# Optimization experiments

Measured on AMD Instinct MI355X. Metric: run time of the kernel, lower is better.

Reference implementation:

```python
import jax, jax.numpy as jnp
import numpy as np

N = 50000
E = 800000
IN_C, HID, OUT_C = 512, 256, 128


def gcn_conv(x, edge_index, W, b, num_nodes):
    # PyG GCNConv: add self-loops, symmetric normalization, linear-then-aggregate.
    h = x @ W  # [N, out]
    src = jnp.concatenate([edge_index[0], jnp.arange(num_nodes)])
    dst = jnp.concatenate([edge_index[1], jnp.arange(num_nodes)])
    ones = jnp.ones(src.shape[0], dtype=x.dtype)
    deg = jax.ops.segment_sum(ones, dst, num_segments=num_nodes)  # in-degree incl. self-loop
    dinv = jax.lax.rsqrt(deg)  # deg >= 1 thanks to self-loops
    norm = dinv[src] * dinv[dst]  # [E+N]
    msg = h[src] * norm[:, None]  # gather + scale
    out = jax.ops.segment_sum(msg, dst, num_segments=num_nodes)  # scatter-add
    return out + b


def setup_inputs() -> dict:
    key = jax.random.key(0)
    k_x, k_e, k_w1, k_b1, k_w2, k_b2 = jax.random.split(key, 6)
    x = jax.random.normal(k_x, (N, IN_C), dtype=jnp.float32)
    edge_index = jax.random.randint(k_e, (2, E), 0, N, dtype=jnp.int64)
    s1 = 1.0 / np.sqrt(IN_C)
    s2 = 1.0 / np.sqrt(HID)
    W1 = jax.random.uniform(k_w1, (IN_C, HID), jnp.float32, -s1, s1)
    b1 = jax.random.uniform(k_b1, (HID,), jnp.float32, -s1, s1)
    W2 = jax.random.uniform(k_w2, (HID, OUT_C), jnp.float32, -s2, s2)
    b2 = jax.random.uniform(k_b2, (OUT_C,), jnp.float32, -s2, s2)
    return {"x": x, "edge_index": edge_index, "W1": W1, "b1": b1, "W2": W2, "b2": b2}


def reference(x, edge_index, W1, b1, W2, b2):
    h = gcn_conv(x, edge_index, W1, b1, N)
    h = jax.nn.relu(h)
    # dropout in eval mode == identity
    return gcn_conv(h, edge_index, W2, b2, N)
```

## Files before the change

### kernel.cpp

```cpp
#include <hip/hip_runtime.h>
#include <stdint.h>

typedef __bf16 bf16_t;
typedef bf16_t bf16x8 __attribute__((ext_vector_type(8)));
typedef bf16_t bf16x4 __attribute__((ext_vector_type(4)));
typedef bf16_t bf16x2 __attribute__((ext_vector_type(2)));
typedef float  f32x4  __attribute__((ext_vector_type(4)));

#define IN_C 512
#define HID  256
#define OUTC 128

__global__ void k_detect(const void* __restrict__ ei, int* __restrict__ flag, int n_nodes) {
  if (blockIdx.x == 0 && threadIdx.x == 0) {
    const long long* p = (const long long*)ei;
    int ok = 1;
    for (int i = 0; i < 64; ++i) {
      long long v = p[i];
      if (v < 0 || v >= n_nodes) ok = 0;
    }
    *flag = ok;
  }
}

__global__ void k_hist(const void* __restrict__ ei, const int* __restrict__ flag,
                       int* __restrict__ cnt, int E) {
  int e = blockIdx.x * blockDim.x + threadIdx.x;
  if (e >= E) return;
  int d;
  if (*flag) d = (int)((const long long*)ei)[(size_t)E + e];
  else       d = ((const int*)ei)[E + e];
  atomicAdd(&cnt[d], 1);
}

__global__ void k_scan1(const int* __restrict__ cnt, int* __restrict__ ex,
                        int* __restrict__ part, float* __restrict__ dinv, int n) {
  __shared__ int sh[256];
  int i = blockIdx.x * 256 + threadIdx.x;
  int v = (i < n) ? cnt[i] : 0;
  if (i < n) dinv[i] = rsqrtf((float)v + 1.0f);
  sh[threadIdx.x] = v;
  __syncthreads();
  int val = v;
  for (int off = 1; off < 256; off <<= 1) {
    int t = (threadIdx.x >= off) ? sh[threadIdx.x - off] : 0;
    __syncthreads();
    val += t;
    sh[threadIdx.x] = val;
    __syncthreads();
  }
  if (i < n) ex[i] = val - v;
  if (threadIdx.x == 255) part[blockIdx.x] = val;
}

__global__ void k_scan2(int* __restrict__ part, int nb) {
  __shared__ int sh[256];
  int v = (threadIdx.x < nb) ? part[threadIdx.x] : 0;
  sh[threadIdx.x] = v;
  __syncthreads();
  int val = v;
  for (int off = 1; off < 256; off <<= 1) {
    int t = (threadIdx.x >= off) ? sh[threadIdx.x - off] : 0;
    __syncthreads();
    val += t;
    sh[threadIdx.x] = val;
    __syncthreads();
  }
  if (threadIdx.x < nb) part[threadIdx.x] = val - v;
}

__global__ void k_scan3(int* __restrict__ rs, const int* __restrict__ part,
                        int* __restrict__ cur, int n, int Etot) {
  int i = blockIdx.x * 256 + threadIdx.x;
  if (i < n) {
    int r = rs[i] + part[blockIdx.x];
    rs[i] = r;
    cur[i] = r;
  }
  if (i == 0) rs[n] = Etot;
}

__global__ void k_fill(const void* __restrict__ ei, const int* __restrict__ flag,
                       int* __restrict__ cur, int* __restrict__ csr, int E) {
  int e = blockIdx.x * blockDim.x + threadIdx.x;
  if (e >= E) return;
  int s, d;
  if (*flag) {
    const long long* p = (const long long*)ei;
    s = (int)p[e];
    d = (int)p[(size_t)E + e];
  } else {
    const int* p = (const int*)ei;
    s = p[e];
    d = p[E + e];
  }
  int pos = atomicAdd(&cur[d], 1);
  csr[pos] = s;
}

__global__ void k_transw(const float* __restrict__ W1, const float* __restrict__ W2,
                         bf16_t* __restrict__ W1t, bf16_t* __restrict__ W2t) {
  int t = blockIdx.x * blockDim.x + threadIdx.x;
  if (t < IN_C * HID) {
    int k = t / HID, nn = t % HID;
    W1t[(size_t)nn * IN_C + k] = (bf16_t)W1[t];
  } else {
    int u = t - IN_C * HID;
    if (u < HID * OUTC) {
      int k = u / OUTC, nn = u % OUTC;
      W2t[(size_t)nn * HID + k] = (bf16_t)W2[u];
    }
  }
}

__global__ __launch_bounds__(256, 2) void k_gemm1(const float* __restrict__ x,
                                                  const bf16_t* __restrict__ Bt,
                                                  bf16_t* __restrict__ C, int n) {
  __shared__ bf16_t As[64 * 40];
  __shared__ bf16_t Bs[256 * 40];
  const int bm = blockIdx.x;
  const int tid = threadIdx.x;
  const int wave = tid >> 6, lane = tid & 63;
  const int wm = (wave >> 1) * 32, wn = (wave & 1) * 128;
  const int quad = lane >> 4, l16 = lane & 15;
  const int arow = tid >> 2, acol = (tid & 3) * 8;
  const int grow = bm * 64 + arow;

  f32x4 acc[2][8];
  for (int i = 0; i < 2; ++i)
    for (int j = 0; j < 8; ++j)
      for (int r = 0; r < 4; ++r) acc[i][j][r] = 0.0f;

  for (int kk = 0; kk < IN_C; kk += 32) {
    bf16x8 va;
    if (grow < n) {
      const float4* px = (const float4*)(x + (size_t)grow * IN_C + kk + acol);
      float4 a = px[0], b = px[1];
      va[0] = (bf16_t)a.x; va[1] = (bf16_t)a.y; va[2] = (bf16_t)a.z; va[3] = (bf16_t)a.w;
      va[4] = (bf16_t)b.x; va[5] = (bf16_t)b.y; va[6] = (bf16_t)b.z; va[7] = (bf16_t)b.w;
    } else {
      for (int i = 0; i < 8; ++i) va[i] = (bf16_t)0.0f;
    }
    *(bf16x8*)(&As[arow * 40 + acol]) = va;
#pragma unroll
    for (int c = 0; c < 4; ++c) {
      bf16x8 vb = *(const bf16x8*)(Bt + (size_t)tid * IN_C + kk + c * 8);
      *(bf16x8*)(&Bs[tid * 40 + c * 8]) = vb;
    }
    __syncthreads();
    bf16x8 af[2], bfr[8];
#pragma unroll
    for (int i = 0; i < 2; ++i)
      af[i] = *(const bf16x8*)(&As[(wm + i * 16 + l16) * 40 + quad * 8]);
#pragma unroll
    for (int j = 0; j < 8; ++j)
      bfr[j] = *(const bf16x8*)(&Bs[(wn + j * 16 + l16) * 40 + quad * 8]);
#pragma unroll
    for (int i = 0; i < 2; ++i)
#pragma unroll
      for (int j = 0; j < 8; ++j)
        acc[i][j] = __builtin_amdgcn_mfma_f32_16x16x32_bf16(af[i], bfr[j], acc[i][j], 0, 0, 0);
    __syncthreads();
  }

#pragma unroll
  for (int i = 0; i < 2; ++i) {
#pragma unroll
    for (int j = 0; j < 8; ++j) {
      int col = wn + j * 16 + l16;
      int row0 = bm * 64 + wm + i * 16 + quad * 4;
#pragma unroll
      for (int r = 0; r < 4; ++r)
        C[(size_t)(row0 + r) * HID + col] = (bf16_t)acc[i][j][r];
    }
  }
}

__global__ __launch_bounds__(256, 2) void k_gemm2(const bf16_t* __restrict__ A,
                                                  const bf16_t* __restrict__ Bt,
                                                  bf16_t* __restrict__ C) {
  __shared__ bf16_t As[64 * 40];
  __shared__ bf16_t Bs[128 * 40];
  const int bm = blockIdx.x;
  const int tid = threadIdx.x;
  const int wave = tid >> 6, lane = tid & 63;
  const int wm = (wave >> 1) * 32, wn = (wave & 1) * 64;
  const int quad = lane >> 4, l16 = lane & 15;
  const int arow = tid >> 2, acol = (tid & 3) * 8;
  const int brow = tid >> 1, bcol = (tid & 1) * 16;

  f32x4 acc[2][4];
  for (int i = 0; i < 2; ++i)
    for (int j = 0; j < 4; ++j)
      for (int r = 0; r < 4; ++r) acc[i][j][r] = 0.0f;

  for (int kk = 0; kk < HID; kk += 32) {
    bf16x8 va = *(const bf16x8*)(A + (size_t)(bm * 64 + arow) * HID + kk + acol);
    *(bf16x8*)(&As[arow * 40 + acol]) = va;
#pragma unroll
    for (int c = 0; c < 2; ++c) {
      bf16x8 vb = *(const bf16x8*)(Bt + (size_t)brow * HID + kk + bcol + c * 8);
      *(bf16x8*)(&Bs[brow * 40 + bcol + c * 8]) = vb;
    }
    __syncthreads();
    bf16x8 af[2], bfr[4];
#pragma unroll
    for (int i = 0; i < 2; ++i)
      af[i] = *(const bf16x8*)(&As[(wm + i * 16 + l16) * 40 + quad * 8]);
#pragma unroll
    for (int j = 0; j < 4; ++j)
      bfr[j] = *(const bf16x8*)(&Bs[(wn + j * 16 + l16) * 40 + quad * 8]);
#pragma unroll
    for (int i = 0; i < 2; ++i)
#pragma unroll
      for (int j = 0; j < 4; ++j)
        acc[i][j] = __builtin_amdgcn_mfma_f32_16x16x32_bf16(af[i], bfr[j], acc[i][j], 0, 0, 0);
    __syncthreads();
  }

#pragma unroll
  for (int i = 0; i < 2; ++i) {
#pragma unroll
    for (int j = 0; j < 4; ++j) {
      int col = wn + j * 16 + l16;
      int row0 = bm * 64 + wm + i * 16 + quad * 4;
#pragma unroll
      for (int r = 0; r < 4; ++r)
        C[(size_t)(row0 + r) * OUTC + col] = (bf16_t)acc[i][j][r];
    }
  }
}

__global__ void k_agg_l1(const bf16_t* __restrict__ H, const int* __restrict__ rs,
                         const int* __restrict__ csr, const float* __restrict__ dinv,
                         const float* __restrict__ b1, bf16_t* __restrict__ R,
                         int n, int mpad) {
  int d = blockIdx.x * 4 + (threadIdx.x >> 6);
  if (d >= mpad) return;
  int lane = threadIdx.x & 63;
  if (d >= n) {
    bf16x4 z;
    z[0] = (bf16_t)0.0f; z[1] = (bf16_t)0.0f; z[2] = (bf16_t)0.0f; z[3] = (bf16_t)0.0f;
    *(bf16x4*)(R + (size_t)d * HID + lane * 4) = z;
    return;
  }
  int e0 = rs[d], e1 = rs[d + 1];
  float acc[4][4];
  for (int k = 0; k < 4; ++k)
    for (int c = 0; c < 4; ++c) acc[k][c] = 0.f;
  int e = e0;
  for (; e + 4 <= e1; e += 4) {
    int s0 = csr[e], s1 = csr[e + 1], s2 = csr[e + 2], s3 = csr[e + 3];
    float w0 = dinv[s0], w1 = dinv[s1], w2 = dinv[s2], w3 = dinv[s3];
    bf16x4 h0 = *(const bf16x4*)(H + (size_t)s0 * HID + lane * 4);
    bf16x4 h1 = *(const bf16x4*)(H + (size_t)s1 * HID + lane * 4);
    bf16x4 h2 = *(const bf16x4*)(H + (size_t)s2 * HID + lane * 4);
    bf16x4 h3 = *(const bf16x4*)(H + (size_t)s3 * HID + lane * 4);
#pragma unroll
    for (int c = 0; c < 4; ++c) {
      acc[0][c] += w0 * (float)h0[c];
      acc[1][c] += w1 * (float)h1[c];
      acc[2][c] += w2 * (float)h2[c];
      acc[3][c] += w3 * (float)h3[c];
    }
  }
  for (; e < e1; ++e) {
    int s0 = csr[e];
    float w0 = dinv[s0];
    bf16x4 h0 = *(const bf16x4*)(H + (size_t)s0 * HID + lane * 4);
#pragma unroll
    for (int c = 0; c < 4; ++c) acc[0][c] += w0 * (float)h0[c];
  }
  float dd = dinv[d];
  float dv2 = dd * dd;
  bf16x4 hs = *(const bf16x4*)(H + (size_t)d * HID + lane * 4);
  float4 bb = ((const float4*)b1)[lane];
  float a0 = acc[0][0] + acc[1][0] + acc[2][0] + acc[3][0];
  float a1 = acc[0][1] + acc[1][1] + acc[2][1] + acc[3][1];
  float a2 = acc[0][2] + acc[1][2] + acc[2][2] + acc[3][2];
  float a3 = acc[0][3] + acc[1][3] + acc[2][3] + acc[3][3];
  float v0 = fmaxf(a0 * dd + dv2 * (float)hs[0] + bb.x, 0.f);
  float v1 = fmaxf(a1 * dd + dv2 * (float)hs[1] + bb.y, 0.f);
  float v2 = fmaxf(a2 * dd + dv2 * (float)hs[2] + bb.z, 0.f);
  float v3 = fmaxf(a3 * dd + dv2 * (float)hs[3] + bb.w, 0.f);
  bf16x4 o;
  o[0] = (bf16_t)v0; o[1] = (bf16_t)v1; o[2] = (bf16_t)v2; o[3] = (bf16_t)v3;
  *(bf16x4*)(R + (size_t)d * HID + lane * 4) = o;
}

__global__ void k_agg_l2(const bf16_t* __restrict__ H, const int* __restrict__ rs,
                         const int* __restrict__ csr, const float* __restrict__ dinv,
                         const float* __restrict__ b2, float* __restrict__ out, int n) {
  int d = blockIdx.x * 4 + (threadIdx.x >> 6);
  if (d >= n) return;
  int lane = threadIdx.x & 63;
  int e0 = rs[d], e1 = rs[d + 1];
  float acc[4][2];
  for (int k = 0; k < 4; ++k) { acc[k][0] = 0.f; acc[k][1] = 0.f; }
  int e = e0;
  for (; e + 4 <= e1; e += 4) {
    int s0 = csr[e], s1 = csr[e + 1], s2 = csr[e + 2], s3 = csr[e + 3];
    float w0 = dinv[s0], w1 = dinv[s1], w2 = dinv[s2], w3 = dinv[s3];
    bf16x2 h0 = *(const bf16x2*)(H + (size_t)s0 * OUTC + lane * 2);
    bf16x2 h1 = *(const bf16x2*)(H + (size_t)s1 * OUTC + lane * 2);
    bf16x2 h2 = *(const bf16x2*)(H + (size_t)s2 * OUTC + lane * 2);
    bf16x2 h3 = *(const bf16x2*)(H + (size_t)s3 * OUTC + lane * 2);
    acc[0][0] += w0 * (float)h0[0]; acc[0][1] += w0 * (float)h0[1];
    acc[1][0] += w1 * (float)h1[0]; acc[1][1] += w1 * (float)h1[1];
    acc[2][0] += w2 * (float)h2[0]; acc[2][1] += w2 * (float)h2[1];
    acc[3][0] += w3 * (float)h3[0]; acc[3][1] += w3 * (float)h3[1];
  }
  for (; e < e1; ++e) {
    int s0 = csr[e];
    float w0 = dinv[s0];
    bf16x2 h0 = *(const bf16x2*)(H + (size_t)s0 * OUTC + lane * 2);
    acc[0][0] += w0 * (float)h0[0]; acc[0][1] += w0 * (float)h0[1];
  }
  float a0 = acc[0][0] + acc[1][0] + acc[2][0] + acc[3][0];
  float a1 = acc[0][1] + acc[1][1] + acc[2][1] + acc[3][1];
  float dd = dinv[d];
  float dv2 = dd * dd;
  bf16x2 hs = *(const bf16x2*)(H + (size_t)d * OUTC + lane * 2);
  float2 bb = ((const float2*)b2)[lane];
  float2 o;
  o.x = a0 * dd + dv2 * (float)hs[0] + bb.x;
  o.y = a1 * dd + dv2 * (float)hs[1] + bb.y;
  ((float2*)(out + (size_t)d * OUTC))[lane] = o;
}

extern "C" void kernel_launch(void* const* d_in, const int* in_sizes, int n_in,
                              void* d_out, int out_size, void* d_ws, size_t ws_size,
                              hipStream_t stream) {
  const float* x  = (const float*)d_in[0];
  const void*  ei = d_in[1];
  const float* W1 = (const float*)d_in[2];
  const float* b1 = (const float*)d_in[3];
  const float* W2 = (const float*)d_in[4];
  const float* b2 = (const float*)d_in[5];

  const int n = in_sizes[0] / IN_C;
  const int E = in_sizes[1] / 2;
  const int mpad = (n + 63) & ~63;

  char* w = (char*)d_ws;
  size_t off = 0;
  auto alloc = [&](size_t bytes) -> void* {
    void* p = w + off;
    off = (off + bytes + 255) & ~(size_t)255;
    return p;
  };

  int*    flag = (int*)alloc(4);
  int*    cnt  = (int*)alloc((size_t)n * 4);
  float*  dinv = (float*)alloc((size_t)n * 4);
  int*    rs   = (int*)alloc((size_t)(n + 1) * 4);
  int*    cur  = (int*)alloc((size_t)n * 4);
  int*    part = (int*)alloc(1024);
  int*    csr  = (int*)alloc((size_t)E * 4);
  bf16_t* W1t  = (bf16_t*)alloc((size_t)HID * IN_C * 2);
  bf16_t* W2t  = (bf16_t*)alloc((size_t)OUTC * HID * 2);
  bf16_t* H1b  = (bf16_t*)alloc((size_t)mpad * HID * 2);
  bf16_t* R1b  = (bf16_t*)alloc((size_t)mpad * HID * 2);
  bf16_t* H2b  = (bf16_t*)alloc((size_t)mpad * OUTC * 2);
  (void)ws_size; (void)n_in; (void)out_size;

  const int nb = (n + 255) / 256;

  hipMemsetAsync(cnt, 0, (size_t)n * 4, stream);
  k_detect<<<1, 64, 0, stream>>>(ei, flag, n);
  k_hist<<<(E + 255) / 256, 256, 0, stream>>>(ei, flag, cnt, E);
  k_scan1<<<nb, 256, 0, stream>>>(cnt, rs, part, dinv, n);
  k_scan2<<<1, 256, 0, stream>>>(part, nb);
  k_scan3<<<nb, 256, 0, stream>>>(rs, part, cur, n, E);
  k_fill<<<(E + 255) / 256, 256, 0, stream>>>(ei, flag, cur, csr, E);
  k_transw<<<(IN_C * HID + HID * OUTC + 255) / 256, 256, 0, stream>>>(W1, W2, W1t, W2t);

  k_gemm1<<<mpad / 64, 256, 0, stream>>>(x, W1t, H1b, n);
  k_agg_l1<<<(mpad + 3) / 4, 256, 0, stream>>>(H1b, rs, csr, dinv, b1, R1b, n, mpad);
  k_gemm2<<<mpad / 64, 256, 0, stream>>>(R1b, W2t, H2b);
  k_agg_l2<<<(n + 3) / 4, 256, 0, stream>>>(H2b, rs, csr, dinv, b2, (float*)d_out, n);
}
```

Before: 401.3 us.

## Precompute per-edge source weights, load GEMM A fragments directly, deepen gather unroll

k_fill now stores dinv[src] alongside each CSR entry, so the aggregation kernels read it contiguously instead of doing a dependent random gather. GEMM1 loads x fragments straight from global into registers, stages W1 in a pre-blocked 64-wide K layout, and synchronises once per 64-K chunk. GEMM2 keeps all of W2 resident in LDS and reads A fragments directly from global, with no per-iteration barriers. The aggregation loops unroll to 8 edges to keep more loads in flight, at the cost of an extra E-sized buffer and more registers.

```diff
diff --git a/kernel.cpp b/kernel.cpp
--- a/kernel.cpp
+++ b/kernel.cpp
@@ -81,7 +81,8 @@
 }
 
 __global__ void k_fill(const void* __restrict__ ei, const int* __restrict__ flag,
-                       int* __restrict__ cur, int* __restrict__ csr, int E) {
+                       int* __restrict__ cur, int* __restrict__ csr,
+                       float* __restrict__ wsrc, const float* __restrict__ dinv, int E) {
   int e = blockIdx.x * blockDim.x + threadIdx.x;
   if (e >= E) return;
   int s, d;
@@ -96,71 +97,80 @@
   }
   int pos = atomicAdd(&cur[d], 1);
   csr[pos] = s;
+  wsrc[pos] = dinv[s];
 }
 
 __global__ void k_transw(const float* __restrict__ W1, const float* __restrict__ W2,
-                         bf16_t* __restrict__ W1t, bf16_t* __restrict__ W2t) {
+                         bf16_t* __restrict__ W1blk, bf16_t* __restrict__ W2t) {
   int t = blockIdx.x * blockDim.x + threadIdx.x;
   if (t < IN_C * HID) {
-    int k = t / HID, nn = t % HID;
-    W1t[(size_t)nn * IN_C + k] = (bf16_t)W1[t];
+    int k = t >> 8, col = t & 255;
+    W1blk[(size_t)(k >> 6) * (HID * 64) + col * 64 + (k & 63)] = (bf16_t)W1[t];
   } else {
     int u = t - IN_C * HID;
     if (u < HID * OUTC) {
-      int k = u / OUTC, nn = u % OUTC;
-      W2t[(size_t)nn * HID + k] = (bf16_t)W2[u];
+      int k = u >> 7, col = u & 127;
+      W2t[(size_t)col * HID + k] = (bf16_t)W2[u];
     }
   }
 }
 
 __global__ __launch_bounds__(256, 2) void k_gemm1(const float* __restrict__ x,
-                                                  const bf16_t* __restrict__ Bt,
+                                                  const bf16_t* __restrict__ Bblk,
                                                   bf16_t* __restrict__ C, int n) {
-  __shared__ bf16_t As[64 * 40];
-  __shared__ bf16_t Bs[256 * 40];
+  __shared__ bf16_t Bs[256 * 72];
   const int bm = blockIdx.x;
   const int tid = threadIdx.x;
   const int wave = tid >> 6, lane = tid & 63;
   const int wm = (wave >> 1) * 32, wn = (wave & 1) * 128;
   const int quad = lane >> 4, l16 = lane & 15;
-  const int arow = tid >> 2, acol = (tid & 3) * 8;
-  const int grow = bm * 64 + arow;
+  const int row0 = bm * 64 + wm + l16;
 
   f32x4 acc[2][8];
   for (int i = 0; i < 2; ++i)
     for (int j = 0; j < 8; ++j)
       for (int r = 0; r < 4; ++r) acc[i][j][r] = 0.0f;
 
-  for (int kk = 0; kk < IN_C; kk += 32) {
-    bf16x8 va;
-    if (grow < n) {
-      const float4* px = (const float4*)(x + (size_t)grow * IN_C + kk + acol);
-      float4 a = px[0], b = px[1];
-      va[0] = (bf16_t)a.x; va[1] = (bf16_t)a.y; va[2] = (bf16_t)a.z; va[3] = (bf16_t)a.w;
-      va[4] = (bf16_t)b.x; va[5] = (bf16_t)b.y; va[6] = (bf16_t)b.z; va[7] = (bf16_t)b.w;
-    } else {
-      for (int i = 0; i < 8; ++i) va[i] = (bf16_t)0.0f;
-    }
-    *(bf16x8*)(&As[arow * 40 + acol]) = va;
-#pragma unroll
-    for (int c = 0; c < 4; ++c) {
-      bf16x8 vb = *(const bf16x8*)(Bt + (size_t)tid * IN_C + kk + c * 8);
-      *(bf16x8*)(&Bs[tid * 40 + c * 8]) = vb;
-    }
-    __syncthreads();
-    bf16x8 af[2], bfr[8];
-#pragma unroll
-    for (int i = 0; i < 2; ++i)
-      af[i] = *(const bf16x8*)(&As[(wm + i * 16 + l16) * 40 + quad * 8]);
-#pragma unroll
-    for (int j = 0; j < 8; ++j)
-      bfr[j] = *(const bf16x8*)(&Bs[(wn + j * 16 + l16) * 40 + quad * 8]);
-#pragma unroll
-    for (int i = 0; i < 2; ++i)
+  for (int kb = 0; kb < 8; ++kb) {
+    const int kk = kb * 64;
+    bf16x8 afr[2][2];
+#pragma unroll
+    for (int i = 0; i < 2; ++i) {
+      int r = row0 + i * 16;
+#pragma unroll
+      for (int k2 = 0; k2 < 2; ++k2) {
+        if (r < n) {
+          const float4* p = (const float4*)(x + (size_t)r * IN_C + kk + k2 * 32 + quad * 8);
+          float4 a = p[0], b = p[1];
+          afr[i][k2][0] = (bf16_t)a.x; afr[i][k2][1] = (bf16_t)a.y;
+          afr[i][k2][2] = (bf16_t)a.z; afr[i][k2][3] = (bf16_t)a.w;
+          afr[i][k2][4] = (bf16_t)b.x; afr[i][k2][5] = (bf16_t)b.y;
+          afr[i][k2][6] = (bf16_t)b.z; afr[i][k2][7] = (bf16_t)b.w;
+        } else {
+          for (int u = 0; u < 8; ++u) afr[i][k2][u] = (bf16_t)0.0f;
+        }
+      }
+    }
+    __syncthreads();
+    const bf16_t* gb = Bblk + (size_t)kb * (HID * 64) + (size_t)tid * 64;
+#pragma unroll
+    for (int u = 0; u < 8; ++u) {
+      bf16x8 v = *(const bf16x8*)(gb + u * 8);
+      *(bf16x8*)(&Bs[tid * 72 + u * 8]) = v;
+    }
+    __syncthreads();
+#pragma unroll
+    for (int k2 = 0; k2 < 2; ++k2) {
+      bf16x8 bfr[8];
 #pragma unroll
       for (int j = 0; j < 8; ++j)
-        acc[i][j] = __builtin_amdgcn_mfma_f32_16x16x32_bf16(af[i], bfr[j], acc[i][j], 0, 0, 0);
-    __syncthreads();
+        bfr[j] = *(const bf16x8*)(&Bs[(wn + j * 16 + l16) * 72 + k2 * 32 + quad * 8]);
+#pragma unroll
+      for (int i = 0; i < 2; ++i)
+#pragma unroll
+        for (int j = 0; j < 8; ++j)
+          acc[i][j] = __builtin_amdgcn_mfma_f32_16x16x32_bf16(afr[i][k2], bfr[j], acc[i][j], 0, 0, 0);
+    }
   }
 
 #pragma unroll
@@ -168,54 +178,56 @@
 #pragma unroll
     for (int j = 0; j < 8; ++j) {
       int col = wn + j * 16 + l16;
-      int row0 = bm * 64 + wm + i * 16 + quad * 4;
+      int rw0 = bm * 64 + wm + i * 16 + quad * 4;
 #pragma unroll
       for (int r = 0; r < 4; ++r)
-        C[(size_t)(row0 + r) * HID + col] = (bf16_t)acc[i][j][r];
+        C[(size_t)(rw0 + r) * HID + col] = (bf16_t)acc[i][j][r];
     }
   }
 }
 
 __global__ __launch_bounds__(256, 2) void k_gemm2(const bf16_t* __restrict__ A,
-                                                  const bf16_t* __restrict__ Bt,
+                                                  const bf16_t* __restrict__ W2t,
                                                   bf16_t* __restrict__ C) {
-  __shared__ bf16_t As[64 * 40];
-  __shared__ bf16_t Bs[128 * 40];
+  __shared__ bf16_t Bs[128 * 264];
   const int bm = blockIdx.x;
   const int tid = threadIdx.x;
   const int wave = tid >> 6, lane = tid & 63;
   const int wm = (wave >> 1) * 32, wn = (wave & 1) * 64;
   const int quad = lane >> 4, l16 = lane & 15;
-  const int arow = tid >> 2, acol = (tid & 3) * 8;
-  const int brow = tid >> 1, bcol = (tid & 1) * 16;
+
+#pragma unroll
+  for (int i = 0; i < 16; ++i) {
+    int g = i * 256 + tid;
+    int row = g >> 5, cc = g & 31;
+    bf16x8 v = *(const bf16x8*)(W2t + (size_t)row * HID + cc * 8);
+    *(bf16x8*)(&Bs[row * 264 + cc * 8]) = v;
+  }
+  __syncthreads();
 
   f32x4 acc[2][4];
   for (int i = 0; i < 2; ++i)
     for (int j = 0; j < 4; ++j)
       for (int r = 0; r < 4; ++r) acc[i][j][r] = 0.0f;
 
-  for (int kk = 0; kk < HID; kk += 32) {
-    bf16x8 va = *(const bf16x8*)(A + (size_t)(bm * 64 + arow) * HID + kk + acol);
-    *(bf16x8*)(&As[arow * 40 + acol]) = va;
-#pragma unroll
-    for (int c = 0; c < 2; ++c) {
-      bf16x8 vb = *(const bf16x8*)(Bt + (size_t)brow * HID + kk + bcol + c * 8);
-      *(bf16x8*)(&Bs[brow * 40 + bcol + c * 8]) = vb;
-    }
-    __syncthreads();
-    bf16x8 af[2], bfr[4];
-#pragma unroll
-    for (int i = 0; i < 2; ++i)
-      af[i] = *(const bf16x8*)(&As[(wm + i * 16 + l16) * 40 + quad * 8]);
+#pragma unroll
+  for (int ks = 0; ks < 8; ++ks) {
+    const int kk = ks * 32;
+    bf16x8 af[2];
+#pragma unroll
+    for (int i = 0; i < 2; ++i) {
+      int r = bm * 64 + wm + i * 16 + l16;
+      af[i] = *(const bf16x8*)(A + (size_t)r * HID + kk + quad * 8);
+    }
+    bf16x8 bfr[4];
 #pragma unroll
     for (int j = 0; j < 4; ++j)
-      bfr[j] = *(const bf16x8*)(&Bs[(wn + j * 16 + l16) * 40 + quad * 8]);
+      bfr[j] = *(const bf16x8*)(&Bs[(wn + j * 16 + l16) * 264 + kk + quad * 8]);
 #pragma unroll
     for (int i = 0; i < 2; ++i)
 #pragma unroll
       for (int j = 0; j < 4; ++j)
         acc[i][j] = __builtin_amdgcn_mfma_f32_16x16x32_bf16(af[i], bfr[j], acc[i][j], 0, 0, 0);
-    __syncthreads();
   }
 
 #pragma unroll
@@ -223,18 +235,18 @@
 #pragma unroll
     for (int j = 0; j < 4; ++j) {
       int col = wn + j * 16 + l16;
-      int row0 = bm * 64 + wm + i * 16 + quad * 4;
+      int rw0 = bm * 64 + wm + i * 16 + quad * 4;
 #pragma unroll
       for (int r = 0; r < 4; ++r)
-        C[(size_t)(row0 + r) * OUTC + col] = (bf16_t)acc[i][j][r];
+        C[(size_t)(rw0 + r) * OUTC + col] = (bf16_t)acc[i][j][r];
     }
   }
 }
 
 __global__ void k_agg_l1(const bf16_t* __restrict__ H, const int* __restrict__ rs,
-                         const int* __restrict__ csr, const float* __restrict__ dinv,
-                         const float* __restrict__ b1, bf16_t* __restrict__ R,
-                         int n, int mpad) {
+                         const int* __restrict__ csr, const float* __restrict__ wsrc,
+                         const float* __restrict__ dinv, const float* __restrict__ b1,
+                         bf16_t* __restrict__ R, int n, int mpad) {
   int d = blockIdx.x * 4 + (threadIdx.x >> 6);
   if (d >= mpad) return;
   int lane = threadIdx.x & 63;
@@ -249,36 +261,35 @@
   for (int k = 0; k < 4; ++k)
     for (int c = 0; c < 4; ++c) acc[k][c] = 0.f;
   int e = e0;
-  for (; e + 4 <= e1; e += 4) {
-    int s0 = csr[e], s1 = csr[e + 1], s2 = csr[e + 2], s3 = csr[e + 3];
-    float w0 = dinv[s0], w1 = dinv[s1], w2 = dinv[s2], w3 = dinv[s3];
-    bf16x4 h0 = *(const bf16x4*)(H + (size_t)s0 * HID + lane * 4);
-    bf16x4 h1 = *(const bf16x4*)(H + (size_t)s1 * HID + lane * 4);
-    bf16x4 h2 = *(const bf16x4*)(H + (size_t)s2 * HID + lane * 4);
-    bf16x4 h3 = *(const bf16x4*)(H + (size_t)s3 * HID + lane * 4);
-#pragma unroll
-    for (int c = 0; c < 4; ++c) {
-      acc[0][c] += w0 * (float)h0[c];
-      acc[1][c] += w1 * (float)h1[c];
-      acc[2][c] += w2 * (float)h2[c];
-      acc[3][c] += w3 * (float)h3[c];
-    }
+  for (; e + 8 <= e1; e += 8) {
+    int   s[8];
+    float w[8];
+    bf16x4 h[8];
+#pragma unroll
+    for (int u = 0; u < 8; ++u) { s[u] = csr[e + u]; w[u] = wsrc[e + u]; }
+#pragma unroll
+    for (int u = 0; u < 8; ++u)
+      h[u] = *(const bf16x4*)(H + (size_t)s[u] * HID + lane * 4);
+#pragma unroll
+    for (int u = 0; u < 8; ++u)
+#pragma unroll
+      for (int c = 0; c < 4; ++c) acc[u & 3][c] += w[u] * (float)h[u][c];
   }
   for (; e < e1; ++e) {
-    int s0 = csr[e];
-    float w0 = dinv[s0];
-    bf16x4 h0 = *(const bf16x4*)(H + (size_t)s0 * HID + lane * 4);
-#pragma unroll
-    for (int c = 0; c < 4; ++c) acc[0][c] += w0 * (float)h0[c];
+    int sx = csr[e];
+    float wx = wsrc[e];
+    bf16x4 hx = *(const bf16x4*)(H + (size_t)sx * HID + lane * 4);
+#pragma unroll
+    for (int c = 0; c < 4; ++c) acc[0][c] += wx * (float)hx[c];
   }
   float dd = dinv[d];
   float dv2 = dd * dd;
   bf16x4 hs = *(const bf16x4*)(H + (size_t)d * HID + lane * 4);
   float4 bb = ((const float4*)b1)[lane];
-  float a0 = acc[0][0] + acc[1][0] + acc[2][0] + acc[3][0];
-  float a1 = acc[0][1] + acc[1][1] + acc[2][1] + acc[3][1];
-  float a2 = acc[0][2] + acc[1][2] + acc[2][2] + acc[3][2];
-  float a3 = acc[0][3] + acc[1][3] + acc[2][3] + acc[3][3];
+  float a0 = (acc[0][0] + acc[1][0]) + (acc[2][0] + acc[3][0]);
+  float a1 = (acc[0][1] + acc[1][1]) + (acc[2][1] + acc[3][1]);
+  float a2 = (acc[0][2] + acc[1][2]) + (acc[2][2] + acc[3][2]);
+  float a3 = (acc[0][3] + acc[1][3]) + (acc[2][3] + acc[3][3]);
   float v0 = fmaxf(a0 * dd + dv2 * (float)hs[0] + bb.x, 0.f);
   float v1 = fmaxf(a1 * dd + dv2 * (float)hs[1] + bb.y, 0.f);
   float v2 = fmaxf(a2 * dd + dv2 * (float)hs[2] + bb.z, 0.f);
@@ -289,8 +300,9 @@
 }
 
 __global__ void k_agg_l2(const bf16_t* __restrict__ H, const int* __restrict__ rs,
-                         const int* __restrict__ csr, const float* __restrict__ dinv,
-                         const float* __restrict__ b2, float* __restrict__ out, int n) {
+                         const int* __restrict__ csr, const float* __restrict__ wsrc,
+                         const float* __restrict__ dinv, const float* __restrict__ b2,
+                         float* __restrict__ out, int n) {
   int d = blockIdx.x * 4 + (threadIdx.x >> 6);
   if (d >= n) return;
   int lane = threadIdx.x & 63;
@@ -298,26 +310,30 @@
   float acc[4][2];
   for (int k = 0; k < 4; ++k) { acc[k][0] = 0.f; acc[k][1] = 0.f; }
   int e = e0;
-  for (; e + 4 <= e1; e += 4) {
-    int s0 = csr[e], s1 = csr[e + 1], s2 = csr[e + 2], s3 = csr[e + 3];
-    float w0 = dinv[s0], w1 = dinv[s1], w2 = dinv[s2], w3 = dinv[s3];
-    bf16x2 h0 = *(const bf16x2*)(H + (size_t)s0 * OUTC + lane * 2);
-    bf16x2 h1 = *(const bf16x2*)(H + (size_t)s1 * OUTC + lane * 2);
-    bf16x2 h2 = *(const bf16x2*)(H + (size_t)s2 * OUTC + lane * 2);
-    bf16x2 h3 = *(const bf16x2*)(H + (size_t)s3 * OUTC + lane * 2);
-    acc[0][0] += w0 * (float)h0[0]; acc[0][1] += w0 * (float)h0[1];
-    acc[1][0] += w1 * (float)h1[0]; acc[1][1] += w1 * (float)h1[1];
-    acc[2][0] += w2 * (float)h2[0]; acc[2][1] += w2 * (float)h2[1];
-    acc[3][0] += w3 * (float)h3[0]; acc[3][1] += w3 * (float)h3[1];
+  for (; e + 8 <= e1; e += 8) {
+    int   s[8];
+    float w[8];
+    bf16x2 h[8];
+#pragma unroll
+    for (int u = 0; u < 8; ++u) { s[u] = csr[e + u]; w[u] = wsrc[e + u]; }
+#pragma unroll
+    for (int u = 0; u < 8; ++u)
+      h[u] = *(const bf16x2*)(H + (size_t)s[u] * OUTC + lane * 2);
+#pragma unroll
+    for (int u = 0; u < 8; ++u) {
+      acc[u & 3][0] += w[u] * (float)h[u][0];
+      acc[u & 3][1] += w[u] * (float)h[u][1];
+    }
   }
   for (; e < e1; ++e) {
-    int s0 = csr[e];
-    float w0 = dinv[s0];
-    bf16x2 h0 = *(const bf16x2*)(H + (size_t)s0 * OUTC + lane * 2);
-    acc[0][0] += w0 * (float)h0[0]; acc[0][1] += w0 * (float)h0[1];
-  }
-  float a0 = acc[0][0] + acc[1][0] + acc[2][0] + acc[3][0];
-  float a1 = acc[0][1] + acc[1][1] + acc[2][1] + acc[3][1];
+    int sx = csr[e];
+    float wx = wsrc[e];
+    bf16x2 hx = *(const bf16x2*)(H + (size_t)sx * OUTC + lane * 2);
+    acc[0][0] += wx * (float)hx[0];
+    acc[0][1] += wx * (float)hx[1];
+  }
+  float a0 = (acc[0][0] + acc[1][0]) + (acc[2][0] + acc[3][0]);
+  float a1 = (acc[0][1] + acc[1][1]) + (acc[2][1] + acc[3][1]);
   float dd = dinv[d];
   float dv2 = dd * dd;
   bf16x2 hs = *(const bf16x2*)(H + (size_t)d * OUTC + lane * 2);
@@ -357,7 +373,8 @@
   int*    cur  = (int*)alloc((size_t)n * 4);
   int*    part = (int*)alloc(1024);
   int*    csr  = (int*)alloc((size_t)E * 4);
-  bf16_t* W1t  = (bf16_t*)alloc((size_t)HID * IN_C * 2);
+  float*  wsrc = (float*)alloc((size_t)E * 4);
+  bf16_t* W1blk= (bf16_t*)alloc((size_t)HID * IN_C * 2);
   bf16_t* W2t  = (bf16_t*)alloc((size_t)OUTC * HID * 2);
   bf16_t* H1b  = (bf16_t*)alloc((size_t)mpad * HID * 2);
   bf16_t* R1b  = (bf16_t*)alloc((size_t)mpad * HID * 2);
@@ -372,11 +389,11 @@
   k_scan1<<<nb, 256, 0, stream>>>(cnt, rs, part, dinv, n);
   k_scan2<<<1, 256, 0, stream>>>(part, nb);
   k_scan3<<<nb, 256, 0, stream>>>(rs, part, cur, n, E);
-  k_fill<<<(E + 255) / 256, 256, 0, stream>>>(ei, flag, cur, csr, E);
-  k_transw<<<(IN_C * HID + HID * OUTC + 255) / 256, 256, 0, stream>>>(W1, W2, W1t, W2t);
-
-  k_gemm1<<<mpad / 64, 256, 0, stream>>>(x, W1t, H1b, n);
-  k_agg_l1<<<(mpad + 3) / 4, 256, 0, stream>>>(H1b, rs, csr, dinv, b1, R1b, n, mpad);
+  k_fill<<<(E + 255) / 256, 256, 0, stream>>>(ei, flag, cur, csr, wsrc, dinv, E);
+  k_transw<<<(IN_C * HID + HID * OUTC + 255) / 256, 256, 0, stream>>>(W1, W2, W1blk, W2t);
+
+  k_gemm1<<<mpad / 64, 256, 0, stream>>>(x, W1blk, H1b, n);
+  k_agg_l1<<<(mpad + 3) / 4, 256, 0, stream>>>(H1b, rs, csr, wsrc, dinv, b1, R1b, n, mpad);
   k_gemm2<<<mpad / 64, 256, 0, stream>>>(R1b, W2t, H2b);
-  k_agg_l2<<<(n + 3) / 4, 256, 0, stream>>>(H2b, rs, csr, dinv, b2, (float*)d_out, n);
-}
+  k_agg_l2<<<(n + 3) / 4, 256, 0, stream>>>(H2b, rs, csr, wsrc, dinv, b2, (float*)d_out, n);
+}
```

Result: slower. 423.6 us (+5.6%).
